# Kernel tuning notes

Measured on AMD Instinct MI355X. Metric: run time of the kernel, lower is better.

## Reference

```python
import jax, jax.numpy as jnp
import numpy as np

D = 1024
H = 16
B = 8
N = 1024


def setup_inputs() -> dict:
    key = jax.random.key(0)
    k1, k2, k3 = jax.random.split(key, 3)
    x = jax.random.normal(k1, (B, N, D), dtype=jnp.float32)
    w_in = jax.random.normal(k2, (D, 3 * D), dtype=jnp.float32) * (1.0 / np.sqrt(D))
    w_out = jax.random.normal(k3, (D, D), dtype=jnp.float32) * (1.0 / np.sqrt(D))
    b_out = jnp.zeros((D,), dtype=jnp.float32)
    return {"x": x, "w_in": w_in, "w_out": w_out, "b_out": b_out}


def reference(x, w_in, w_out, b_out):
    h = H
    d = D // H
    scale = D ** (-0.5)  # note: full dimension, per source
    qkv = x @ w_in  # [B, N, 3D]
    # rearrange 'b n (qkv h d) -> qkv b h n d'
    qkv = qkv.reshape(x.shape[0], x.shape[1], 3, h, d)
    qkv = jnp.transpose(qkv, (2, 0, 3, 1, 4))
    q, k, v = qkv[0], qkv[1], qkv[2]
    scores = jnp.einsum('bhid,bhjd->bhij', q, k) * scale
    attn = jax.nn.softmax(scores, axis=-1)
    out = jnp.einsum('bhij,bhjd->bhid', attn, v)
    # 'b h n d -> b n (h d)'
    out = jnp.transpose(out, (0, 2, 1, 3)).reshape(x.shape[0], x.shape[1], h * d)
    return out @ w_out + b_out
```

## Files before the change

kernel.cpp:

```cpp
#include <hip/hip_runtime.h>
#include <stdint.h>
#include <stddef.h>

typedef __bf16 bf16;
typedef __bf16 bf16x4 __attribute__((ext_vector_type(4)));
typedef __bf16 bf16x8 __attribute__((ext_vector_type(8)));
typedef float  f32x4  __attribute__((ext_vector_type(4)));
typedef float  f32x16 __attribute__((ext_vector_type(16)));
typedef float  f32x4v __attribute__((ext_vector_type(4)));

__device__ __forceinline__ void gload_lds16(const void* g, void* lds) {
  __builtin_amdgcn_global_load_lds(
      (__attribute__((address_space(1))) void*)(uintptr_t)g,
      (__attribute__((address_space(3))) void*)lds,
      16, 0, 0);
}


__global__ void cvt_f32_to_bf16(const float* __restrict__ in, bf16* __restrict__ out, int n) {
  int i = (blockIdx.x * blockDim.x + threadIdx.x) * 4;
  if (i >= n) return;
  f32x4v v = *reinterpret_cast<const f32x4v*>(in + i);
  bf16x4 o;
  o[0] = (bf16)v[0]; o[1] = (bf16)v[1]; o[2] = (bf16)v[2]; o[3] = (bf16)v[3];
  *reinterpret_cast<bf16x4*>(out + i) = o;
}

__global__ void transpose_cvt(const float* __restrict__ in, bf16* __restrict__ out, int R, int C) {
  __shared__ bf16 tile[32][33];
  int c0 = blockIdx.x * 32, r0 = blockIdx.y * 32;
  int tx = threadIdx.x, ty = threadIdx.y;
  #pragma unroll
  for (int i = ty; i < 32; i += 8)
    tile[i][tx] = (bf16)in[(size_t)(r0 + i) * C + (c0 + tx)];
  __syncthreads();
  #pragma unroll
  for (int i = ty; i < 32; i += 8)
    out[(size_t)(c0 + i) * R + (r0 + tx)] = tile[tx][i];
}


template <typename OT, bool BIAS>
__global__ __launch_bounds__(256) void gemm_abt(
    const bf16* __restrict__ A,
    const bf16* __restrict__ Bt,
    const float* __restrict__ bias,
    OT* __restrict__ C, int M, int N, int K)
{
  __shared__ bf16 As[128 * 64];
  __shared__ bf16 Bs[128 * 64];

  const int tid = threadIdx.x;
  const int w = tid >> 6, l = tid & 63;
  const int l15 = l & 15, l4 = l >> 4, l7 = l & 7;
  const int wr = w >> 1, wc = w & 1;
  const int m0 = blockIdx.y * 128, n0 = blockIdx.x * 128;

  f32x4 acc[4][4];
  #pragma unroll
  for (int i = 0; i < 4; i++)
    #pragma unroll
    for (int j = 0; j < 4; j++) acc[i][j] = (f32x4){0.f, 0.f, 0.f, 0.f};

  const int srow  = w * 8 + (l >> 3);
  const int sslot = (l & 7) ^ ((l >> 3) & 7);
  const int KT = K >> 6;

  for (int kt = 0; kt < KT; ++kt) {
    __syncthreads();
    const int kcol = kt * 64 + sslot * 8;
    #pragma unroll
    for (int p = 0; p < 4; ++p) {
      gload_lds16(A  + (size_t)(m0 + p * 32 + srow) * K + kcol,
                  (char*)As + p * 4096 + w * 1024);
      gload_lds16(Bt + (size_t)(n0 + p * 32 + srow) * K + kcol,
                  (char*)Bs + p * 4096 + w * 1024);
    }
    __syncthreads();

    #pragma unroll
    for (int kk = 0; kk < 2; ++kk) {
      const int coff = (kk * 32 + l4 * 8) ^ (l7 << 3);
      bf16x8 af[4], bq[4];
      #pragma unroll
      for (int m = 0; m < 4; ++m) {
        int r = wr * 64 + m * 16 + l15;
        af[m] = *reinterpret_cast<const bf16x8*>(&As[r * 64 + coff]);
      }
      #pragma unroll
      for (int n = 0; n < 4; ++n) {
        int r = wc * 64 + n * 16 + l15;
        bq[n] = *reinterpret_cast<const bf16x8*>(&Bs[r * 64 + coff]);
      }
      #pragma unroll
      for (int m = 0; m < 4; ++m)
        #pragma unroll
        for (int n = 0; n < 4; ++n)
          acc[m][n] = __builtin_amdgcn_mfma_f32_16x16x32_bf16(af[m], bq[n], acc[m][n], 0, 0, 0);
    }
  }

  #pragma unroll
  for (int m = 0; m < 4; ++m) {
    #pragma unroll
    for (int n = 0; n < 4; ++n) {
      int col = n0 + wc * 64 + n * 16 + l15;
      float bv = BIAS ? bias[col] : 0.f;
      #pragma unroll
      for (int j = 0; j < 4; ++j) {
        int row = m0 + wr * 64 + m * 16 + l4 * 4 + j;
        float v = acc[m][n][j] + bv;
        C[(size_t)row * N + col] = (OT)v;
      }
    }
  }
}


__global__ __launch_bounds__(256) void attn_fused(
    const bf16* __restrict__ qkv,
    bf16* __restrict__ aout)
{
  __shared__ bf16 Ks[64 * 64];
  __shared__ bf16 Vt[64 * 64];
  __shared__ bf16 Pl[4][32 * 64];

  const int tid = threadIdx.x;
  const int w = tid >> 6, l = tid & 63;
  const int l31 = l & 31, hi = l >> 5;

  const int bid = blockIdx.x;
  const int c  = bid & 7, rr = bid >> 3;
  const int g  = c * 16 + (rr & 15);
  const int qt = rr >> 4;
  const int h  = g & 15;
  const int b  = g >> 4;

  const bf16* base = qkv + (size_t)b * 1024 * 3072;
  const int qrow0 = qt * 128 + w * 32;

  const float qscale = 0.03125f * 1.44269504f;
  bf16x8 qf[4];
  #pragma unroll
  for (int st = 0; st < 4; st++) {
    const bf16* p = base + (size_t)(qrow0 + l31) * 3072 + h * 64 + st * 16 + hi * 8;
    bf16x8 v = *reinterpret_cast<const bf16x8*>(p);
    #pragma unroll
    for (int e = 0; e < 8; e++) v[e] = (bf16)((float)v[e] * qscale);
    qf[st] = v;
  }

  bf16x8 onesf;
  #pragma unroll
  for (int e = 0; e < 8; e++) onesf[e] = (bf16)1.0f;

  f32x16 acc0 = {}, acc1 = {}, accS = {};

  const int skey  = w * 8 + (l >> 3);
  const int sslot = (l & 7) ^ ((l >> 3) & 7);
  const int vd0   = (tid & 15) * 4;
  const int vk0   = (tid >> 4) * 4;
  const int vslot = tid >> 5;
  const int vhalf = (tid >> 4) & 1;

  for (int kt = 0; kt < 16; ++kt) {
    __syncthreads();
    #pragma unroll
    for (int p = 0; p < 2; ++p)
      gload_lds16(base + (size_t)(kt * 64 + p * 32 + skey) * 3072 + 1024 + h * 64 + sslot * 8,
                  (char*)Ks + p * 4096 + w * 1024);
    {
      bf16x4 vv[4];
      #pragma unroll
      for (int i = 0; i < 4; ++i)
        vv[i] = *reinterpret_cast<const bf16x4*>(
            base + (size_t)(kt * 64 + vk0 + i) * 3072 + 2048 + h * 64 + vd0);
      #pragma unroll
      for (int j = 0; j < 4; ++j) {
        int d = vd0 + j;
        bf16x4 o; o[0] = vv[0][j]; o[1] = vv[1][j]; o[2] = vv[2][j]; o[3] = vv[3][j];
        *reinterpret_cast<bf16x4*>(
            &Vt[d * 64 + ((vslot ^ (d & 7) ^ ((d >> 3) & 7)) * 8 + vhalf * 4)]) = o;
      }
    }
    __syncthreads();

    #pragma unroll
    for (int ktile = 0; ktile < 2; ++ktile) {
      f32x16 s = {};
      const int key = ktile * 32 + l31;
      #pragma unroll
      for (int st = 0; st < 4; ++st) {
        const int slot = (2 * st + hi) ^ (key & 7);
        bf16x8 kf = *reinterpret_cast<const bf16x8*>(&Ks[key * 64 + slot * 8]);
        s = __builtin_amdgcn_mfma_f32_32x32x16_bf16(kf, qf[st], s, 0, 0, 0);
      }
      #pragma unroll
      for (int gq = 0; gq < 4; ++gq) {
        bf16x4 pb;
        #pragma unroll
        for (int j2 = 0; j2 < 4; ++j2) {
          float pv = __builtin_amdgcn_exp2f(s[4 * gq + j2]);
          pb[j2] = (bf16)pv;
        }
        const int chunk = ktile * 4 + gq;
        *reinterpret_cast<bf16x4*>(
            &Pl[w][l31 * 64 + ((chunk ^ (l31 & 7)) * 8 + hi * 4)]) = pb;
      }
    }

    const int d7x0 = (l31 & 7) ^ (l31 >> 3);
    const int d7x1 = d7x0 ^ 4;
    #pragma unroll
    for (int st = 0; st < 4; ++st) {
      const int cs = 2 * st + hi;
      bf16x8 pa  = *reinterpret_cast<const bf16x8*>(
          &Pl[w][l31 * 64 + ((cs ^ (l31 & 7)) * 8)]);
      accS = __builtin_amdgcn_mfma_f32_32x32x16_bf16(pa, onesf, accS, 0, 0, 0);
      bf16x8 vf0 = *reinterpret_cast<const bf16x8*>(
          &Vt[l31 * 64 + ((cs ^ d7x0) * 8)]);
      acc0 = __builtin_amdgcn_mfma_f32_32x32x16_bf16(pa, vf0, acc0, 0, 0, 0);
      bf16x8 vf1 = *reinterpret_cast<const bf16x8*>(
          &Vt[(32 + l31) * 64 + ((cs ^ d7x1) * 8)]);
      acc1 = __builtin_amdgcn_mfma_f32_32x32x16_bf16(pa, vf1, acc1, 0, 0, 0);
    }
  }

  #pragma unroll
  for (int reg = 0; reg < 16; ++reg) {
    int q_r = (reg & 3) + 8 * (reg >> 2) + 4 * hi;
    float rinv = 1.0f / accS[reg];
    size_t rowoff = ((size_t)b * 1024 + qrow0 + q_r) * 1024 + h * 64;
    aout[rowoff + l31]      = (bf16)(acc0[reg] * rinv);
    aout[rowoff + 32 + l31] = (bf16)(acc1[reg] * rinv);
  }
}


extern "C" void kernel_launch(void* const* d_in, const int* in_sizes, int n_in,
                              void* d_out, int out_size, void* d_ws, size_t ws_size,
                              hipStream_t stream) {
  const float* x     = (const float*)d_in[0];
  const float* w_in  = (const float*)d_in[1];
  const float* w_out = (const float*)d_in[2];
  const float* b_out = (const float*)d_in[3];
  float* out = (float*)d_out;

  bf16* xb    = (bf16*)d_ws;
  bf16* wint  = xb    + (size_t)8192 * 1024;
  bf16* woutt = wint  + (size_t)3072 * 1024;
  bf16* qkv   = woutt + (size_t)1024 * 1024;
  bf16* ao    = qkv   + (size_t)8192 * 3072;

  cvt_f32_to_bf16<<<8192, 256, 0, stream>>>(x, xb, 8192 * 1024);
  transpose_cvt<<<dim3(96, 32), dim3(32, 8), 0, stream>>>(w_in,  wint,  1024, 3072);
  transpose_cvt<<<dim3(32, 32), dim3(32, 8), 0, stream>>>(w_out, woutt, 1024, 1024);

  gemm_abt<bf16, false><<<dim3(24, 64), 256, 0, stream>>>(xb, wint, nullptr, qkv, 8192, 3072, 1024);

  attn_fused<<<1024, 256, 0, stream>>>(qkv, ao);

  gemm_abt<float, true><<<dim3(8, 64), 256, 0, stream>>>(ao, woutt, b_out, out, 8192, 1024, 1024);
}
```

Measured before the change: 173.1 us.

## Add double-buffered 256x256 8-wave GEMM for QKV projection

Introduces a new GEMM kernel with 512 threads and 256x256 tiles, double-buffered LDS and prefetch of the next K tile interleaved with MFMA phases, plus XCD-aware block swizzling and s_setprio around the MFMA bursts. It replaces the 128x128 single-buffered GEMM for the QKV projection, aiming to hide global-load latency and raise data reuse per tile. Costs include 128KB LDS per block and large accumulator register use, which limit occupancy to one block per CU.

New measurement: 171.7 us. Within noise of the previous version (-0.8%).

```diff
diff --git a/kernel.cpp b/kernel.cpp
--- a/kernel.cpp
+++ b/kernel.cpp
@@ -110,6 +110,129 @@
       for (int j = 0; j < 4; ++j) {
         int row = m0 + wr * 64 + m * 16 + l4 * 4 + j;
         float v = acc[m][n][j] + bv;
+        C[(size_t)row * N + col] = (OT)v;
+      }
+    }
+  }
+}
+
+
+template <typename OT, bool BIAS>
+__global__ __launch_bounds__(512) void gemm_abt8(
+    const bf16* __restrict__ A,
+    const bf16* __restrict__ Bt,
+    const float* __restrict__ bias,
+    OT* __restrict__ C, int M, int N, int K)
+{
+  __shared__ bf16 As[2][256 * 64];
+  __shared__ bf16 Bs[2][256 * 64];
+
+  const int tid = threadIdx.x;
+  const int w = tid >> 6, l = tid & 63;
+  const int l15 = l & 15, l4 = l >> 4, l7 = l & 7;
+  const int wm = w >> 2, wn = w & 3;
+
+  const int nwgx = N >> 8;
+  const int nwg  = (M >> 8) * nwgx;
+  const int cpx  = nwg >> 3;
+  const int bid  = blockIdx.x;
+  const int swz  = (bid & 7) * cpx + (bid >> 3);
+  const int m0 = (swz / nwgx) * 256, n0 = (swz % nwgx) * 256;
+
+  f32x4 acc[8][4];
+  #pragma unroll
+  for (int i = 0; i < 8; i++)
+    #pragma unroll
+    for (int j = 0; j < 4; j++) acc[i][j] = (f32x4){0.f, 0.f, 0.f, 0.f};
+
+  const int w8l   = w * 8 + (l >> 3);
+  const int sslot = (l & 7) ^ ((l >> 3) & 7);
+  const int KT = K >> 6;
+
+  {
+    const int kcol = sslot * 8;
+    #pragma unroll
+    for (int p = 0; p < 4; ++p) {
+      gload_lds16(A  + (size_t)(m0 + p * 64 + w8l) * K + kcol,
+                  (char*)As[0] + p * 8192 + w * 1024);
+      gload_lds16(Bt + (size_t)(n0 + p * 64 + w8l) * K + kcol,
+                  (char*)Bs[0] + p * 8192 + w * 1024);
+    }
+  }
+  asm volatile("s_waitcnt vmcnt(0)" ::: "memory");
+  __builtin_amdgcn_s_barrier();
+
+  for (int t = 0; t < KT; ++t) {
+    const int cur = t & 1, nxt = cur ^ 1;
+    const bf16* as = As[cur];
+    const bf16* bs = Bs[cur];
+    const int kcol = (t + 1) * 64 + sslot * 8;
+    const bool pre = (t < KT - 1);
+
+    bf16x8 afr[4][2];
+    bf16x8 bfr[2][2];
+
+    #pragma unroll
+    for (int ph = 0; ph < 4; ++ph) {
+      const int mh = ph >> 1, nh = ph & 1;
+
+      if (nh == 0) {
+        #pragma unroll
+        for (int i = 0; i < 4; ++i)
+          #pragma unroll
+          for (int kk = 0; kk < 2; ++kk)
+            afr[i][kk] = *reinterpret_cast<const bf16x8*>(
+                &as[wm * 8192 + ((mh * 4 + i) * 16 + l15) * 64 + (((kk * 4 + l4) ^ l7) * 8)]);
+      }
+      #pragma unroll
+      for (int n2 = 0; n2 < 2; ++n2)
+        #pragma unroll
+        for (int kk = 0; kk < 2; ++kk)
+          bfr[n2][kk] = *reinterpret_cast<const bf16x8*>(
+              &bs[(wn >> 1) * 8192 + ((wn & 1) * 64 + (nh * 2 + n2) * 16 + l15) * 64
+                  + (((kk * 4 + l4) ^ l7) * 8)]);
+
+      if (pre && ph == 0) {
+        #pragma unroll
+        for (int p = 0; p < 4; ++p)
+          gload_lds16(A + (size_t)(m0 + p * 64 + w8l) * K + kcol,
+                      (char*)As[nxt] + p * 8192 + w * 1024);
+      }
+      if (pre && ph == 1) {
+        #pragma unroll
+        for (int p = 0; p < 4; ++p)
+          gload_lds16(Bt + (size_t)(n0 + p * 64 + w8l) * K + kcol,
+                      (char*)Bs[nxt] + p * 8192 + w * 1024);
+      }
+
+      __builtin_amdgcn_s_barrier();
+      __builtin_amdgcn_s_setprio(1);
+      #pragma unroll
+      for (int i = 0; i < 4; ++i)
+        #pragma unroll
+        for (int n2 = 0; n2 < 2; ++n2)
+          #pragma unroll
+          for (int kk = 0; kk < 2; ++kk)
+            acc[mh * 4 + i][nh * 2 + n2] = __builtin_amdgcn_mfma_f32_16x16x32_bf16(
+                afr[i][kk], bfr[n2][kk], acc[mh * 4 + i][nh * 2 + n2], 0, 0, 0);
+      __builtin_amdgcn_s_setprio(0);
+      if (ph == 3) {
+        asm volatile("s_waitcnt vmcnt(0)" ::: "memory");
+      }
+      __builtin_amdgcn_s_barrier();
+    }
+  }
+
+  #pragma unroll
+  for (int mf = 0; mf < 8; ++mf) {
+    #pragma unroll
+    for (int nf = 0; nf < 4; ++nf) {
+      int col = n0 + wn * 64 + nf * 16 + l15;
+      float bv = BIAS ? bias[col] : 0.f;
+      #pragma unroll
+      for (int j = 0; j < 4; ++j) {
+        int row = m0 + wm * 128 + mf * 16 + l4 * 4 + j;
+        float v = acc[mf][nf][j] + bv;
         C[(size_t)row * N + col] = (OT)v;
       }
     }
@@ -256,7 +379,7 @@
   transpose_cvt<<<dim3(96, 32), dim3(32, 8), 0, stream>>>(w_in,  wint,  1024, 3072);
   transpose_cvt<<<dim3(32, 32), dim3(32, 8), 0, stream>>>(w_out, woutt, 1024, 1024);
 
-  gemm_abt<bf16, false><<<dim3(24, 64), 256, 0, stream>>>(xb, wint, nullptr, qkv, 8192, 3072, 1024);
+  gemm_abt8<bf16, false><<<dim3(384), 512, 0, stream>>>(xb, wint, nullptr, qkv, 8192, 3072, 1024);
 
   attn_fused<<<1024, 256, 0, stream>>>(qkv, ao);
 
```
